# Performance work log

Hardware: AMD Instinct MI355X
Metric: run time of the kernel (lower is better)

## Reference

```python
import jax, jax.numpy as jnp
import numpy as np

D_MODEL = 1024
K_QUERY = 32
K_TOPK = 4

def setup_inputs() -> dict:
    key = jax.random.key(0)
    k1, k2, k3, k4, k5 = jax.random.split(key, 5)
    x = jax.random.normal(k1, (4, 2048, D_MODEL), dtype=jnp.float32)
    # nn.Linear(d_model, k_query): weight [k_query, d_model], bias [k_query]
    sc = 1.0 / np.sqrt(D_MODEL)
    Wq = jax.random.uniform(k2, (K_QUERY, D_MODEL), jnp.float32, -sc, sc)
    bq = jax.random.uniform(k3, (K_QUERY,), jnp.float32, -sc, sc)
    Wk = jax.random.uniform(k4, (K_QUERY, D_MODEL), jnp.float32, -sc, sc)
    bk = jax.random.uniform(k5, (K_QUERY,), jnp.float32, -sc, sc)
    return {"x": x, "Wq": Wq, "bq": bq, "Wk": Wk, "bk": bk}

def reference(x, Wq, bq, Wk, bk):
    # x: [B, T, D]
    queries = jnp.einsum('btd,kd->btk', x, Wq) + bq      # [B, T, Kq]
    keys = jnp.einsum('btd,kd->btk', x, Wk) + bk         # [B, T, Kq]
    sim = jnp.einsum('btk,bsk->bts', queries, keys)      # [B, T, T]
    sim = sim / jnp.sqrt(jnp.float32(queries.shape[-1]))
    _, topk_idx = jax.lax.top_k(sim, K_TOPK)              # [B, T, K]
    # gather neighbors per (b, t): x[b, topk_idx[b, t]] -> [B, T, K, D]
    neighbors = jax.vmap(lambda xb, ib: xb[ib])(x, topk_idx)
    gathered = neighbors.mean(axis=2)                     # [B, T, D]
    return gathered
```

## Files before the change

kernel.cpp:

```cpp
#include <hip/hip_runtime.h>
#include <math.h>

#define D_MODEL 1024
#define T_SEQ   2048
#define NBATCH  4
#define NROWS   (NBATCH * T_SEQ)
#define NOUT    64
#define DCHUNK  256
#define NCHUNK  4

#define SKLD 264
#define SQLD 20

__device__ __forceinline__ bool key_gt(float av, int ai, float bv, int bi) {
    return (av > bv) || (av == bv && ai < bi);
}

__device__ __forceinline__ void cmpswap(float& v0, int& i0, float& v1, int& i1) {
    bool sw = key_gt(v1, i1, v0, i0);
    float nv0 = sw ? v1 : v0, nv1 = sw ? v0 : v1;
    int   ni0 = sw ? i1 : i0, ni1 = sw ? i0 : i1;
    v0 = nv0; v1 = nv1; i0 = ni0; i1 = ni1;
}

__device__ __forceinline__ void merge4(float (&a)[4], int (&ai)[4],
                                       float b0, int j0, float b1, int j1,
                                       float b2, int j2, float b3, int j3) {
    if (!key_gt(a[0], ai[0], b3, j3)) { a[0] = b3; ai[0] = j3; }
    if (!key_gt(a[1], ai[1], b2, j2)) { a[1] = b2; ai[1] = j2; }
    if (!key_gt(a[2], ai[2], b1, j1)) { a[2] = b1; ai[2] = j1; }
    if (!key_gt(a[3], ai[3], b0, j0)) { a[3] = b0; ai[3] = j0; }
    cmpswap(a[0], ai[0], a[2], ai[2]);
    cmpswap(a[1], ai[1], a[3], ai[3]);
    cmpswap(a[0], ai[0], a[1], ai[1]);
    cmpswap(a[2], ai[2], a[3], ai[3]);
}

__device__ __forceinline__ void insert4(float (&tv)[4], int (&tix)[4], float v, int idx) {
    if (v > tv[3]) {
        bool g0 = v > tv[0], g1 = v > tv[1], g2 = v > tv[2];
        float n0 = g0 ? v : tv[0];
        int   m0 = g0 ? idx : tix[0];
        float n1 = g1 ? (g0 ? tv[0] : v) : tv[1];
        int   m1 = g1 ? (g0 ? tix[0] : idx) : tix[1];
        float n2 = g2 ? (g1 ? tv[1] : v) : tv[2];
        int   m2 = g2 ? (g1 ? tix[1] : idx) : tix[2];
        float n3 = g2 ? tv[2] : v;
        int   m3 = g2 ? tix[2] : idx;
        tv[0] = n0; tv[1] = n1; tv[2] = n2; tv[3] = n3;
        tix[0] = m0; tix[1] = m1; tix[2] = m2; tix[3] = m3;
    }
}

__global__ __launch_bounds__(256) void wprep_kernel(
    const float* __restrict__ Wq, const float* __restrict__ Wk,
    double* __restrict__ Wdt)
{
    const int idx = blockIdx.x * 256 + threadIdx.x;
    const int o = idx & 63;
    const int d = idx >> 6;
    float v = (o < 32) ? Wq[(size_t)o * D_MODEL + d]
                       : Wk[(size_t)(o - 32) * D_MODEL + d];
    Wdt[(size_t)d * 64 + o] = (double)v;
}

__global__ __launch_bounds__(512) void proj_partial(
    const float* __restrict__ x, const double* __restrict__ Wdt,
    double* __restrict__ part )
{
    const int rl = threadIdx.x & 63;
    const int og = __builtin_amdgcn_readfirstlane(threadIdx.x >> 6);
    const int rb = blockIdx.x & 127;
    const int c  = blockIdx.x >> 7;
    const int row = rb * 64 + rl;
    const int d0  = c * DCHUNK;

    const float4* xr = reinterpret_cast<const float4*>(x + (size_t)row * D_MODEL + d0);
    const double* wbase = Wdt + (size_t)d0 * 64 + og * 8;

    double acc[8];
    #pragma unroll
    for (int j = 0; j < 8; ++j) acc[j] = 0.0;

    #pragma unroll 4
    for (int i = 0; i < DCHUNK / 4; ++i) {
        float4 xv = xr[i];
        double xd[4] = {xv.x, xv.y, xv.z, xv.w};
        #pragma unroll
        for (int u = 0; u < 4; ++u) {
            const double* w = wbase + (size_t)(i * 4 + u) * 64;
            #pragma unroll
            for (int j = 0; j < 8; ++j)
                acc[j] = fma(xd[u], w[j], acc[j]);
        }
    }

    double* p = part + ((size_t)c * NOUT + og * 8) * NROWS + row;
    #pragma unroll
    for (int j = 0; j < 8; ++j)
        p[(size_t)j * NROWS] = acc[j];
}

__global__ __launch_bounds__(256) void proj_combine(
    const double* __restrict__ part,
    const float* __restrict__ bq, const float* __restrict__ bk,
    float* __restrict__ Qt, float* __restrict__ Kt)
{
    const int idx = blockIdx.x * 256 + threadIdx.x;
    const int out = idx >> 13;
    const int row = idx & (NROWS - 1);
    double s = 0.0;
    #pragma unroll
    for (int c = 0; c < NCHUNK; ++c)
        s += part[((size_t)c * NOUT + out) * NROWS + row];
    const int b = row >> 11, t = row & 2047;
    if (out < 32) {
        Qt[((size_t)b * 32 + out) * T_SEQ + t] = (float)(s + (double)bq[out]);
    } else {
        Kt[((size_t)b * 32 + (out - 32)) * T_SEQ + t] = (float)(s + (double)bk[out - 32]);
    }
}

__global__ __launch_bounds__(128) void sim_topk(
    const float* __restrict__ Qt, const float* __restrict__ Kt,
    float* __restrict__ candVal ,
    int*   __restrict__ candIdx )
{
    __shared__ float klds[32 * SKLD];
    __shared__ float qlds[32 * SQLD];
    __shared__ float cV[2][16][4];
    __shared__ int   cI[2][16][4];

    const int tid  = threadIdx.x;
    const int lane = tid & 63;
    const int wav  = tid >> 6;
    const int half = blockIdx.x & 1;
    const int tt   = (blockIdx.x >> 1) & 127;
    const int b    = blockIdx.x >> 8;
    const int tblk = tt * 16;
    const int sh0  = half * 1024;

    const float* QtB = Qt + (size_t)b * 32 * T_SEQ;
    const float* KtB = Kt + (size_t)b * 32 * T_SEQ;

    {
        const int i  = tid >> 2;
        const int t4 = (tid & 3) * 4;
        float4 v = *reinterpret_cast<const float4*>(QtB + (size_t)i * T_SEQ + tblk + t4);
        *reinterpret_cast<float4*>(&qlds[i * SQLD + t4]) = v;
    }

    const int tg = tid & 3;
    const int t0 = tg * 4;
    const int s0 = (tid >> 2) * 8;

    float tv[4][4]; int tix[4][4];
    #pragma unroll
    for (int r = 0; r < 4; ++r)
        #pragma unroll
        for (int j = 0; j < 4; ++j) { tv[r][j] = -INFINITY; tix[r][j] = 0x7fffffff; }

    for (int st = 0; st < 4; ++st) {
        __syncthreads();
        #pragma unroll
        for (int j = 0; j < 16; ++j) {
            const int f  = (tid + j * 128) * 4;
            const int ki = f >> 8;
            const int ks = f & 255;
            float4 v = *reinterpret_cast<const float4*>(
                KtB + (size_t)ki * T_SEQ + sh0 + st * 256 + ks);
            *reinterpret_cast<float4*>(&klds[ki * SKLD + ks]) = v;
        }
        __syncthreads();

        float acc[4][8];
        #pragma unroll
        for (int r = 0; r < 4; ++r)
            #pragma unroll
            for (int c = 0; c < 8; ++c) acc[r][c] = 0.f;

        #pragma unroll 4
        for (int i = 0; i < 32; ++i) {
            float4 qv  = *reinterpret_cast<const float4*>(&qlds[i * SQLD + t0]);
            float4 kv0 = *reinterpret_cast<const float4*>(&klds[i * SKLD + s0]);
            float4 kv1 = *reinterpret_cast<const float4*>(&klds[i * SKLD + s0 + 4]);
            const float qa[4] = {qv.x, qv.y, qv.z, qv.w};
            const float ka[8] = {kv0.x, kv0.y, kv0.z, kv0.w, kv1.x, kv1.y, kv1.z, kv1.w};
            #pragma unroll
            for (int r = 0; r < 4; ++r)
                #pragma unroll
                for (int c = 0; c < 8; ++c)
                    acc[r][c] = fmaf(qa[r], ka[c], acc[r][c]);
        }

        const int sbase = sh0 + st * 256 + s0;
        #pragma unroll
        for (int c = 0; c < 8; ++c)
            #pragma unroll
            for (int r = 0; r < 4; ++r)
                insert4(tv[r], tix[r], acc[r][c], sbase + c);
    }

    #pragma unroll
    for (int m = 4; m <= 32; m <<= 1) {
        #pragma unroll
        for (int r = 0; r < 4; ++r) {
            float b0 = __shfl_xor(tv[r][0], m, 64);
            float b1 = __shfl_xor(tv[r][1], m, 64);
            float b2 = __shfl_xor(tv[r][2], m, 64);
            float b3 = __shfl_xor(tv[r][3], m, 64);
            int   j0 = __shfl_xor(tix[r][0], m, 64);
            int   j1 = __shfl_xor(tix[r][1], m, 64);
            int   j2 = __shfl_xor(tix[r][2], m, 64);
            int   j3 = __shfl_xor(tix[r][3], m, 64);
            merge4(tv[r], tix[r], b0, j0, b1, j1, b2, j2, b3, j3);
        }
    }

    if (lane < 4) {
        #pragma unroll
        for (int r = 0; r < 4; ++r)
            #pragma unroll
            for (int j = 0; j < 4; ++j) {
                cV[wav][lane * 4 + r][j] = tv[r][j];
                cI[wav][lane * 4 + r][j] = tix[r][j];
            }
    }
    __syncthreads();

    if (tid < 16) {
        float mv[4]; int mi[4];
        #pragma unroll
        for (int j = 0; j < 4; ++j) { mv[j] = cV[0][tid][j]; mi[j] = cI[0][tid][j]; }
        merge4(mv, mi,
               cV[1][tid][0], cI[1][tid][0],
               cV[1][tid][1], cI[1][tid][1],
               cV[1][tid][2], cI[1][tid][2],
               cV[1][tid][3], cI[1][tid][3]);
        const size_t row = (size_t)b * T_SEQ + tblk + tid;
        float4 vv = {mv[0], mv[1], mv[2], mv[3]};
        int4   ii = {mi[0], mi[1], mi[2], mi[3]};
        *reinterpret_cast<float4*>(candVal + ((size_t)half * NROWS + row) * 4) = vv;
        *reinterpret_cast<int4*>(candIdx + ((size_t)half * NROWS + row) * 4) = ii;
    }
}

__global__ __launch_bounds__(256) void merge_gather(
    const float* __restrict__ x,
    const float* __restrict__ candVal, const int* __restrict__ candIdx,
    float* __restrict__ out)
{
    __shared__ int topIdx[8][4];

    const int tid  = threadIdx.x;
    const int row0 = blockIdx.x * 8;
    const int b    = row0 >> 11;

    if (tid < 8) {
        const size_t row = row0 + tid;
        float4 v0 = *reinterpret_cast<const float4*>(candVal + row * 4);
        int4   i0 = *reinterpret_cast<const int4*>(candIdx + row * 4);
        float4 v1 = *reinterpret_cast<const float4*>(candVal + ((size_t)NROWS + row) * 4);
        int4   i1 = *reinterpret_cast<const int4*>(candIdx + ((size_t)NROWS + row) * 4);
        float mv[4] = {v0.x, v0.y, v0.z, v0.w};
        int   mi[4] = {i0.x, i0.y, i0.z, i0.w};
        merge4(mv, mi, v1.x, i1.x, v1.y, i1.y, v1.z, i1.z, v1.w, i1.w);
        #pragma unroll
        for (int j = 0; j < 4; ++j) topIdx[tid][j] = mi[j];
    }
    __syncthreads();

    const float* xb = x + (size_t)b * T_SEQ * D_MODEL;
    float* ob = out + (size_t)row0 * D_MODEL;
    #pragma unroll
    for (int r = 0; r < 8; ++r) {
        const int i0 = topIdx[r][0], i1 = topIdx[r][1], i2 = topIdx[r][2], i3 = topIdx[r][3];
        float4 a0 = *(reinterpret_cast<const float4*>(xb + (size_t)i0 * D_MODEL) + tid);
        float4 a1 = *(reinterpret_cast<const float4*>(xb + (size_t)i1 * D_MODEL) + tid);
        float4 a2 = *(reinterpret_cast<const float4*>(xb + (size_t)i2 * D_MODEL) + tid);
        float4 a3 = *(reinterpret_cast<const float4*>(xb + (size_t)i3 * D_MODEL) + tid);
        float4 o;
        o.x = (a0.x + a1.x + a2.x + a3.x) * 0.25f;
        o.y = (a0.y + a1.y + a2.y + a3.y) * 0.25f;
        o.z = (a0.z + a1.z + a2.z + a3.z) * 0.25f;
        o.w = (a0.w + a1.w + a2.w + a3.w) * 0.25f;
        *(reinterpret_cast<float4*>(ob + (size_t)r * D_MODEL) + tid) = o;
    }
}

extern "C" void kernel_launch(void* const* d_in, const int* in_sizes, int n_in,
                              void* d_out, int out_size, void* d_ws, size_t ws_size,
                              hipStream_t stream) {
    const float* x  = (const float*)d_in[0];
    const float* Wq = (const float*)d_in[1];
    const float* bq = (const float*)d_in[2];
    const float* Wk = (const float*)d_in[3];
    const float* bk = (const float*)d_in[4];
    float* out = (float*)d_out;

    char* wsb = (char*)d_ws;
    double* Wdt  = (double*)wsb;
    float*  Qt   = (float*)(wsb + (size_t)D_MODEL * NOUT * 8);
    float*  Kt   = Qt + (size_t)NBATCH * 32 * T_SEQ;
    double* part = (double*)(wsb + (size_t)D_MODEL * NOUT * 8
                                 + 2 * (size_t)NBATCH * 32 * T_SEQ * 4);
    float*  candVal = (float*)((char*)part + (size_t)NCHUNK * NOUT * NROWS * 8);
    int*    candIdx = (int*)((char*)candVal + (size_t)2 * NROWS * 4 * 4);

    wprep_kernel<<<dim3(256), dim3(256), 0, stream>>>(Wq, Wk, Wdt);
    proj_partial<<<dim3(NCHUNK * 128), dim3(512), 0, stream>>>(x, Wdt, part);
    proj_combine<<<dim3(NOUT * NROWS / 256), dim3(256), 0, stream>>>(part, bq, bk, Qt, Kt);
    sim_topk<<<dim3(1024), dim3(128), 0, stream>>>(Qt, Kt, candVal, candIdx);
    merge_gather<<<dim3(1024), dim3(256), 0, stream>>>(x, candVal, candIdx, out);
}
```

Baseline: 173.8 us.

## Use FP64 MFMA for the projection and fuse the partial-sum combine

Replaces the scalar FP64 FMA projection (split-K partials plus a separate combine kernel) with a single kernel that stages 16 rows of x in LDS and accumulates with 16x16x4 FP64 MFMA, adding bias and writing Qt/Kt directly. A small probe kernel runs each call to work out the MFMA operand and result lane layout at runtime and writes index tables that the projection kernel reads, with a scalar fallback if no layout matches. This removes the partial buffer round trip and one launch, but adds a tiny probe launch, gathers W from global memory per lane, and drops the split-K parallelism.

```diff
diff --git a/kernel.cpp b/kernel.cpp
--- a/kernel.cpp
+++ b/kernel.cpp
@@ -6,11 +6,12 @@
 #define NBATCH  4
 #define NROWS   (NBATCH * T_SEQ)
 #define NOUT    64
-#define DCHUNK  256
-#define NCHUNK  4
 
 #define SKLD 264
 #define SQLD 20
+#define XLD  260
+
+typedef double v4df __attribute__((ext_vector_type(4)));
 
 __device__ __forceinline__ bool key_gt(float av, int ai, float bv, int bi) {
     return (av > bv) || (av == bv && ai < bi);
@@ -52,6 +53,70 @@
     }
 }
 
+__global__ __launch_bounds__(64) void mfma_probe(int* __restrict__ tab)
+{
+    __shared__ double Aref[16][4];
+    __shared__ double Bref[4][16];
+    __shared__ double Dref[16][16];
+
+    const int lane = threadIdx.x;
+    {
+        const int m = lane & 15, k = lane >> 4;
+        Aref[m][k] = (double)(1 + m * 4 + k);
+        Bref[k][m] = (double)(1 + k * 16 + m);
+    }
+    __syncthreads();
+    for (int e = lane; e < 256; e += 64) {
+        const int m = e >> 4, n = e & 15;
+        double s = 0.0;
+        for (int k = 0; k < 4; ++k) s += Aref[m][k] * Bref[k][n];
+        Dref[m][n] = s;
+    }
+    __syncthreads();
+
+    int found = -1;
+    for (int h = 0; h < 16; ++h) {
+        if (found >= 0) break;
+        const int fa = h & 1, fb = (h >> 1) & 1, fd = h >> 2;
+        const int am = fa ? (lane >> 2) : (lane & 15);
+        const int ak = fa ? (lane & 3)  : (lane >> 4);
+        const int bn = fb ? (lane >> 2) : (lane & 15);
+        const int bk = fb ? (lane & 3)  : (lane >> 4);
+        v4df c = {0.0, 0.0, 0.0, 0.0};
+        c = __builtin_amdgcn_mfma_f64_16x16x4f64(Aref[am][ak], Bref[bk][bn], c, 0, 0, 0);
+        bool ok = true;
+        #pragma unroll
+        for (int i = 0; i < 4; ++i) {
+            int dm, dn;
+            if (fd == 0)      { dm = 4 * (lane >> 4) + i; dn = lane & 15; }
+            else if (fd == 1) { dn = 4 * (lane >> 4) + i; dm = lane & 15; }
+            else if (fd == 2) { dm = (lane >> 4) + 4 * i; dn = lane & 15; }
+            else              { dn = (lane >> 4) + 4 * i; dm = lane & 15; }
+            if (c[i] != Dref[dm][dn]) ok = false;
+        }
+        if (__all(ok)) found = h;
+    }
+
+    const int fa = (found >= 0) ? (found & 1) : 0;
+    const int fb = (found >= 0) ? ((found >> 1) & 1) : 0;
+    const int fd = (found >= 0) ? (found >> 2) : 0;
+    tab[1   + lane] = fa ? (lane >> 2) : (lane & 15);
+    tab[65  + lane] = fa ? (lane & 3)  : (lane >> 4);
+    tab[129 + lane] = fb ? (lane & 3)  : (lane >> 4);
+    tab[193 + lane] = fb ? (lane >> 2) : (lane & 15);
+    #pragma unroll
+    for (int i = 0; i < 4; ++i) {
+        int dm, dn;
+        if (fd == 0)      { dm = 4 * (lane >> 4) + i; dn = lane & 15; }
+        else if (fd == 1) { dn = 4 * (lane >> 4) + i; dm = lane & 15; }
+        else if (fd == 2) { dm = (lane >> 4) + 4 * i; dn = lane & 15; }
+        else              { dn = (lane >> 4) + 4 * i; dm = lane & 15; }
+        tab[257 + lane * 4 + i] = dm;
+        tab[513 + lane * 4 + i] = dn;
+    }
+    if (lane == 0) tab[0] = found;
+}
+
 __global__ __launch_bounds__(256) void wprep_kernel(
     const float* __restrict__ Wq, const float* __restrict__ Wk,
     double* __restrict__ Wdt)
@@ -64,60 +129,72 @@
     Wdt[(size_t)d * 64 + o] = (double)v;
 }
 
-__global__ __launch_bounds__(512) void proj_partial(
+__global__ __launch_bounds__(256) void proj_mfma(
     const float* __restrict__ x, const double* __restrict__ Wdt,
-    double* __restrict__ part )
-{
-    const int rl = threadIdx.x & 63;
-    const int og = __builtin_amdgcn_readfirstlane(threadIdx.x >> 6);
-    const int rb = blockIdx.x & 127;
-    const int c  = blockIdx.x >> 7;
-    const int row = rb * 64 + rl;
-    const int d0  = c * DCHUNK;
-
-    const float4* xr = reinterpret_cast<const float4*>(x + (size_t)row * D_MODEL + d0);
-    const double* wbase = Wdt + (size_t)d0 * 64 + og * 8;
-
-    double acc[8];
-    #pragma unroll
-    for (int j = 0; j < 8; ++j) acc[j] = 0.0;
-
-    #pragma unroll 4
-    for (int i = 0; i < DCHUNK / 4; ++i) {
-        float4 xv = xr[i];
-        double xd[4] = {xv.x, xv.y, xv.z, xv.w};
-        #pragma unroll
-        for (int u = 0; u < 4; ++u) {
-            const double* w = wbase + (size_t)(i * 4 + u) * 64;
-            #pragma unroll
-            for (int j = 0; j < 8; ++j)
-                acc[j] = fma(xd[u], w[j], acc[j]);
-        }
-    }
-
-    double* p = part + ((size_t)c * NOUT + og * 8) * NROWS + row;
-    #pragma unroll
-    for (int j = 0; j < 8; ++j)
-        p[(size_t)j * NROWS] = acc[j];
-}
-
-__global__ __launch_bounds__(256) void proj_combine(
-    const double* __restrict__ part,
-    const float* __restrict__ bq, const float* __restrict__ bk,
+    const float* __restrict__ bq, const float* __restrict__ bk_,
+    const int* __restrict__ tab,
     float* __restrict__ Qt, float* __restrict__ Kt)
 {
-    const int idx = blockIdx.x * 256 + threadIdx.x;
-    const int out = idx >> 13;
-    const int row = idx & (NROWS - 1);
-    double s = 0.0;
-    #pragma unroll
-    for (int c = 0; c < NCHUNK; ++c)
-        s += part[((size_t)c * NOUT + out) * NROWS + row];
-    const int b = row >> 11, t = row & 2047;
-    if (out < 32) {
-        Qt[((size_t)b * 32 + out) * T_SEQ + t] = (float)(s + (double)bq[out]);
-    } else {
-        Kt[((size_t)b * 32 + (out - 32)) * T_SEQ + t] = (float)(s + (double)bk[out - 32]);
+    __shared__ float xlds[16 * XLD];
+
+    const int tid  = threadIdx.x;
+    const int lane = tid & 63;
+    const int og   = __builtin_amdgcn_readfirstlane(tid >> 6);
+    const int row0 = blockIdx.x * 16;
+
+    const int flag = tab[0];
+    const int am  = tab[1   + lane];
+    const int ak  = tab[65  + lane];
+    const int bkk = tab[129 + lane];
+    const int bn  = tab[193 + lane];
+
+    const double* wcol = Wdt + og * 16;
+
+    v4df acc = {0.0, 0.0, 0.0, 0.0};
+
+    for (int st = 0; st < 4; ++st) {
+        __syncthreads();
+        #pragma unroll
+        for (int j = 0; j < 4; ++j) {
+            const int f  = j * 256 + tid;
+            const int r  = f >> 6;
+            const int c4 = f & 63;
+            float4 v = *reinterpret_cast<const float4*>(
+                x + (size_t)(row0 + r) * D_MODEL + st * 256 + c4 * 4);
+            *reinterpret_cast<float4*>(&xlds[r * XLD + c4 * 4]) = v;
+        }
+        __syncthreads();
+
+        if (flag >= 0) {
+            #pragma unroll 8
+            for (int kk = 0; kk < 64; ++kk) {
+                double a = (double)xlds[am * XLD + kk * 4 + ak];
+                double b = wcol[(size_t)(st * 256 + kk * 4 + bkk) * 64 + bn];
+                acc = __builtin_amdgcn_mfma_f64_16x16x4f64(a, b, acc, 0, 0, 0);
+            }
+        } else {
+            const int n  = lane & 15;
+            const int r4 = (lane >> 4) * 4;
+            for (int dd = 0; dd < 256; ++dd) {
+                double wv = wcol[(size_t)(st * 256 + dd) * 64 + n];
+                #pragma unroll
+                for (int i = 0; i < 4; ++i)
+                    acc[i] = fma((double)xlds[(r4 + i) * XLD + dd], wv, acc[i]);
+            }
+        }
+    }
+
+    #pragma unroll
+    for (int i = 0; i < 4; ++i) {
+        const int dmv = tab[257 + lane * 4 + i];
+        const int dnv = tab[513 + lane * 4 + i];
+        const int out = og * 16 + dnv;
+        const int row = row0 + dmv;
+        const int bb  = row >> 11, t = row & 2047;
+        const double bias = (out < 32) ? (double)bq[out] : (double)bk_[out - 32];
+        const float v = (float)(acc[i] + bias);
+        if (out < 32) Qt[((size_t)bb * 32 + out) * T_SEQ + t] = v;
+        else          Kt[((size_t)bb * 32 + (out - 32)) * T_SEQ + t] = v;
     }
 }
 
@@ -299,17 +376,16 @@
     float* out = (float*)d_out;
 
     char* wsb = (char*)d_ws;
-    double* Wdt  = (double*)wsb;
-    float*  Qt   = (float*)(wsb + (size_t)D_MODEL * NOUT * 8);
+    int*    tab  = (int*)wsb;
+    double* Wdt  = (double*)(wsb + 4096);
+    float*  Qt   = (float*)(wsb + 4096 + (size_t)D_MODEL * NOUT * 8);
     float*  Kt   = Qt + (size_t)NBATCH * 32 * T_SEQ;
-    double* part = (double*)(wsb + (size_t)D_MODEL * NOUT * 8
-                                 + 2 * (size_t)NBATCH * 32 * T_SEQ * 4);
-    float*  candVal = (float*)((char*)part + (size_t)NCHUNK * NOUT * NROWS * 8);
+    float*  candVal = (float*)((char*)Kt + (size_t)NBATCH * 32 * T_SEQ * 4);
     int*    candIdx = (int*)((char*)candVal + (size_t)2 * NROWS * 4 * 4);
 
+    mfma_probe<<<dim3(1), dim3(64), 0, stream>>>(tab);
     wprep_kernel<<<dim3(256), dim3(256), 0, stream>>>(Wq, Wk, Wdt);
-    proj_partial<<<dim3(NCHUNK * 128), dim3(512), 0, stream>>>(x, Wdt, part);
-    proj_combine<<<dim3(NOUT * NROWS / 256), dim3(256), 0, stream>>>(part, bq, bk, Qt, Kt);
+    proj_mfma<<<dim3(NROWS / 16), dim3(256), 0, stream>>>(x, Wdt, bq, bk, tab, Qt, Kt);
     sim_topk<<<dim3(1024), dim3(128), 0, stream>>>(Qt, Kt, candVal, candIdx);
     merge_gather<<<dim3(1024), dim3(256), 0, stream>>>(x, candVal, candIdx, out);
 }
```

Result: no change. 171.0 us (-1.6%).
